# Kernel optimization log

Hardware: AMD Instinct MI355X
Metric: run time of the kernel (lower is better)

The kernel has to match this reference:

```python
import jax, jax.numpy as jnp
import numpy as np

EPS = 1e-7  # Keras K.epsilon()


def setup_inputs() -> dict:
    key = jax.random.key(0)
    k_x, k_w, k_b, k_u = jax.random.split(key, 4)
    B, T, D, A = 256, 512, 256, 50
    x = jax.random.normal(k_x, (B, T, D), dtype=jnp.float32)
    # Keras initializers.get('normal') -> stddev 0.05 RandomNormal
    W = jax.random.normal(k_w, (D, A), dtype=jnp.float32) * 0.05
    b = jax.random.normal(k_b, (A,), dtype=jnp.float32) * 0.05
    u = jax.random.normal(k_u, (A, 1), dtype=jnp.float32) * 0.05
    return {"x": x, "W": W, "b": b, "u": u}


def reference(x, W, b, u):
    # uit: [B, T, A]
    uit = jnp.tanh(jnp.einsum('btd,da->bta', x, W) + b)
    # ait: [B, T] raw scores -> exp-normalize (as in original, no max-subtract)
    ait = jnp.einsum('bta,a->bt', uit, u[:, 0])
    ait = jnp.exp(ait)
    ait = ait / (jnp.sum(ait, axis=1, keepdims=True) + EPS)
    # weighted pool over time: [B, D]
    return jnp.einsum('btd,bt->bd', x, ait)
```

## Files before the change

### kernel.cpp

```cpp
#include <hip/hip_runtime.h>
#include <hip/hip_bf16.h>
#include <math.h>

#define B_  256
#define T_  512
#define D_  256
#define A_  50
#define EPS 1e-7f
#define NW  16

typedef short  short8  __attribute__((ext_vector_type(8)));
typedef float  floatx4 __attribute__((ext_vector_type(4)));

__device__ inline unsigned short f2bf(float f) {
    unsigned int u = __float_as_uint(f);
    u = (u + 0x7fffu + ((u >> 16) & 1u)) >> 16;
    return (unsigned short)u;
}

__global__ void prep_kernel(const float* __restrict__ W,
                            const float* __restrict__ bias,
                            const float* __restrict__ u,
                            unsigned short* __restrict__ Wf,
                            float* __restrict__ bu64)
{
    int idx = blockIdx.x * 256 + threadIdx.x;
    int j  = idx & 7;
    int l  = (idx >> 3) & 63;
    int ks = (idx >> 9) & 7;
    int nt = idx >> 12;
    int n  = nt * 16 + (l & 15);
    int k  = ks * 32 + (l >> 4) * 8 + j;
    float val = (n < A_) ? W[k * A_ + n] : 0.0f;
    Wf[idx] = f2bf(val);
    if (idx < 64) {
        bu64[idx]      = (idx < A_) ? bias[idx] : 0.0f;
        bu64[64 + idx] = (idx < A_) ? u[idx]    : 0.0f;
    }
}

__device__ inline void pack_bf4(short8& av, int base, float fx, float fy,
                                float fz, float fw)
{
    union { __hip_bfloat162 h2; int i; } c0, c1;
    c0.h2 = __float22bfloat162_rn(make_float2(fx, fy));
    c1.h2 = __float22bfloat162_rn(make_float2(fz, fw));
    av[base + 0] = (short)(c0.i & 0xffff);
    av[base + 1] = (short)((unsigned)c0.i >> 16);
    av[base + 2] = (short)(c1.i & 0xffff);
    av[base + 3] = (short)((unsigned)c1.i >> 16);
}

__device__ inline float4 shflxor4(float4 v, int m) {
    return make_float4(__shfl_xor(v.x, m), __shfl_xor(v.y, m),
                       __shfl_xor(v.z, m), __shfl_xor(v.w, m));
}
__device__ inline float4 add4(float4 a, float4 b) {
    return make_float4(a.x + b.x, a.y + b.y, a.z + b.z, a.w + b.w);
}
__device__ inline float4 sel4(bool p, float4 a, float4 b) {
    return make_float4(p ? a.x : b.x, p ? a.y : b.y,
                       p ? a.z : b.z, p ? a.w : b.w);
}
__device__ inline float4 mul4s(float4 a, float s) {
    return make_float4(a.x * s, a.y * s, a.z * s, a.w * s);
}

__global__ __launch_bounds__(1024)
void fused_kernel(const float* __restrict__ x,
                  const unsigned short* __restrict__ Wf,
                  const float* __restrict__ bu64,
                  float* __restrict__ out)
{
    __shared__ int4  Wl[2048];
    __shared__ float s_lds[T_];
    __shared__ float part[NW * 256];
    __shared__ float s_inv;

    const int tid  = threadIdx.x;
    const int w    = tid >> 6;
    const int l    = tid & 63;
    const int c    = l & 15;
    const int quad = l >> 4;
    const int bb   = blockIdx.x;

    {
        const int4* __restrict__ wsrc = (const int4*)Wf;
        Wl[tid]        = wsrc[tid];
        Wl[tid + 1024] = wsrc[tid + 1024];
    }

    const float*  __restrict__ xb  = x + (size_t)bb * T_ * D_;
    const short8* __restrict__ wl8 = (const short8*)Wl;

    float bnc[4], unc[4];
    #pragma unroll
    for (int nt = 0; nt < 4; nt++) {
        bnc[nt] = bu64[nt * 16 + c];
        unc[nt] = bu64[64 + nt * 16 + c];
    }
    __syncthreads();

    float4 accp = make_float4(0.f, 0.f, 0.f, 0.f);

    #pragma unroll
    for (int t = 0; t < 2; t++) {
        const int rowbase = w * 32 + t * 16;
        const float4* __restrict__ xr =
            (const float4*)(xb + (size_t)(rowbase + c) * D_);

        floatx4 acc[4];
        #pragma unroll
        for (int nt = 0; nt < 4; nt++) acc[nt] = (floatx4){0.f, 0.f, 0.f, 0.f};

        #pragma unroll
        for (int ks = 0; ks < 8; ks++) {
            const float4 a0 = xr[8 * ks + 2 * quad];
            const float4 a1 = xr[8 * ks + 2 * quad + 1];
            short8 av;
            pack_bf4(av, 0, a0.x, a0.y, a0.z, a0.w);
            pack_bf4(av, 4, a1.x, a1.y, a1.z, a1.w);
            #pragma unroll
            for (int nt = 0; nt < 4; nt++) {
                const short8 bv = wl8[(nt * 8 + ks) * 64 + l];
                acc[nt] = __builtin_amdgcn_mfma_f32_16x16x32_bf16(av, bv, acc[nt], 0, 0, 0);
            }
        }

        #pragma unroll
        for (int r = 0; r < 4; r++) {
            float v = 0.0f;
            #pragma unroll
            for (int nt = 0; nt < 4; nt++)
                v += tanhf(acc[nt][r] + bnc[nt]) * unc[nt];
            #pragma unroll
            for (int off = 1; off < 16; off <<= 1)
                v += __shfl_xor(v, off, 16);
            if (c == 0)
                s_lds[rowbase + quad * 4 + r] = expf(v);
        }

        const float ec = s_lds[rowbase + c];

        float4 h8[8];
        #pragma unroll
        for (int j = 0; j < 8; j++) {
            const int o = (j >> 1) * 8 + quad * 2 + (j & 1);
            const float4 a = mul4s(xr[o],      ec);
            const float4 b = mul4s(xr[o + 32], ec);
            h8[j] = add4(sel4((c & 8) != 0, b, a),
                         shflxor4(sel4((c & 8) != 0, a, b), 8));
        }
        float4 h4[4];
        #pragma unroll
        for (int j = 0; j < 4; j++) {
            const float4 a = h4[0], bqq = h4[0];
            (void)a; (void)bqq;
            const float4 aa = h8[j], bb = h8[j + 4];
            h4[j] = add4(sel4((c & 4) != 0, bb, aa),
                         shflxor4(sel4((c & 4) != 0, aa, bb), 4));
        }
        float4 h2[2];
        #pragma unroll
        for (int j = 0; j < 2; j++) {
            const float4 aa = h4[j], bb = h4[j + 2];
            h2[j] = add4(sel4((c & 2) != 0, bb, aa),
                         shflxor4(sel4((c & 2) != 0, aa, bb), 2));
        }
        {
            const float4 aa = h2[0], bb = h2[1];
            const float4 h1 = add4(sel4((c & 1) != 0, bb, aa),
                                   shflxor4(sel4((c & 1) != 0, aa, bb), 1));
            accp = add4(accp, h1);
        }
    }

    const int g = (c >> 1) * 8 + quad * 2 + (c & 1);
    *(float4*)&part[w * 256 + g * 4] = accp;
    __syncthreads();

    if (tid < 64) {
        float s = 0.0f;
        #pragma unroll
        for (int k = 0; k < 8; k++) s += s_lds[tid + k * 64];
        #pragma unroll
        for (int off = 1; off < 64; off <<= 1) s += __shfl_xor(s, off);
        if (tid == 0) s_inv = 1.0f / (s + EPS);
    }
    __syncthreads();

    if (tid < 256) {
        float o = 0.0f;
        #pragma unroll
        for (int wv = 0; wv < NW; wv++) o += part[wv * 256 + tid];
        out[(size_t)bb * 256 + tid] = o * s_inv;
    }
}

extern "C" void kernel_launch(void* const* d_in, const int* in_sizes, int n_in,
                              void* d_out, int out_size, void* d_ws, size_t ws_size,
                              hipStream_t stream)
{
    const float* x = (const float*)d_in[0];
    const float* W = (const float*)d_in[1];
    const float* b = (const float*)d_in[2];
    const float* u = (const float*)d_in[3];

    unsigned short* Wf  = (unsigned short*)d_ws;
    float*         bu64 = (float*)(Wf + 16384);
    float*         out  = (float*)d_out;

    prep_kernel  <<<64,  256,  0, stream>>>(W, b, u, Wf, bu64);
    fused_kernel <<<B_,  1024, 0, stream>>>(x, Wf, bu64, out);
}
```

Baseline: 206.7 us.

## Split each batch row across two blocks with a combine kernel

The fused kernel now launches 512 blocks, each handling half of the time axis (256 rows) of one batch element. It writes the partial pooled vector and partial exp-sum to workspace. A new combine kernel adds the two halves and normalises. This is meant to raise occupancy and parallelism across the GPU's compute units (256 blocks left many idle), at the cost of an extra launch and a workspace round trip.

```diff
diff --git a/kernel.cpp b/kernel.cpp
--- a/kernel.cpp
+++ b/kernel.cpp
@@ -70,12 +70,12 @@
 void fused_kernel(const float* __restrict__ x,
                   const unsigned short* __restrict__ Wf,
                   const float* __restrict__ bu64,
-                  float* __restrict__ out)
+                  float* __restrict__ pp,
+                  float* __restrict__ ps)
 {
     __shared__ int4  Wl[2048];
-    __shared__ float s_lds[T_];
+    __shared__ float s_lds[256];
     __shared__ float part[NW * 256];
-    __shared__ float s_inv;
 
     const int tid  = threadIdx.x;
     const int w    = tid >> 6;
@@ -83,6 +83,8 @@
     const int c    = l & 15;
     const int quad = l >> 4;
     const int bb   = blockIdx.x;
+    const int bat  = bb >> 1;
+    const int half = bb & 1;
 
     {
         const int4* __restrict__ wsrc = (const int4*)Wf;
@@ -90,7 +92,7 @@
         Wl[tid + 1024] = wsrc[tid + 1024];
     }
 
-    const float*  __restrict__ xb  = x + (size_t)bb * T_ * D_;
+    const float*  __restrict__ xb  = x + (size_t)bat * T_ * D_;
     const short8* __restrict__ wl8 = (const short8*)Wl;
 
     float bnc[4], unc[4];
@@ -101,78 +103,71 @@
     }
     __syncthreads();
 
-    float4 accp = make_float4(0.f, 0.f, 0.f, 0.f);
-
-    #pragma unroll
-    for (int t = 0; t < 2; t++) {
-        const int rowbase = w * 32 + t * 16;
-        const float4* __restrict__ xr =
-            (const float4*)(xb + (size_t)(rowbase + c) * D_);
-
-        floatx4 acc[4];
-        #pragma unroll
-        for (int nt = 0; nt < 4; nt++) acc[nt] = (floatx4){0.f, 0.f, 0.f, 0.f};
-
-        #pragma unroll
-        for (int ks = 0; ks < 8; ks++) {
-            const float4 a0 = xr[8 * ks + 2 * quad];
-            const float4 a1 = xr[8 * ks + 2 * quad + 1];
-            short8 av;
-            pack_bf4(av, 0, a0.x, a0.y, a0.z, a0.w);
-            pack_bf4(av, 4, a1.x, a1.y, a1.z, a1.w);
-            #pragma unroll
-            for (int nt = 0; nt < 4; nt++) {
-                const short8 bv = wl8[(nt * 8 + ks) * 64 + l];
-                acc[nt] = __builtin_amdgcn_mfma_f32_16x16x32_bf16(av, bv, acc[nt], 0, 0, 0);
-            }
+    const int rowbase = w * 16;
+    const float4* __restrict__ xr =
+        (const float4*)(xb + (size_t)(half * 256 + rowbase + c) * D_);
+
+    floatx4 acc[4];
+    #pragma unroll
+    for (int nt = 0; nt < 4; nt++) acc[nt] = (floatx4){0.f, 0.f, 0.f, 0.f};
+
+    #pragma unroll
+    for (int ks = 0; ks < 8; ks++) {
+        const float4 a0 = xr[8 * ks + 2 * quad];
+        const float4 a1 = xr[8 * ks + 2 * quad + 1];
+        short8 av;
+        pack_bf4(av, 0, a0.x, a0.y, a0.z, a0.w);
+        pack_bf4(av, 4, a1.x, a1.y, a1.z, a1.w);
+        #pragma unroll
+        for (int nt = 0; nt < 4; nt++) {
+            const short8 bv = wl8[(nt * 8 + ks) * 64 + l];
+            acc[nt] = __builtin_amdgcn_mfma_f32_16x16x32_bf16(av, bv, acc[nt], 0, 0, 0);
         }
-
-        #pragma unroll
-        for (int r = 0; r < 4; r++) {
-            float v = 0.0f;
-            #pragma unroll
-            for (int nt = 0; nt < 4; nt++)
-                v += tanhf(acc[nt][r] + bnc[nt]) * unc[nt];
-            #pragma unroll
-            for (int off = 1; off < 16; off <<= 1)
-                v += __shfl_xor(v, off, 16);
-            if (c == 0)
-                s_lds[rowbase + quad * 4 + r] = expf(v);
-        }
-
-        const float ec = s_lds[rowbase + c];
-
-        float4 h8[8];
-        #pragma unroll
-        for (int j = 0; j < 8; j++) {
-            const int o = (j >> 1) * 8 + quad * 2 + (j & 1);
-            const float4 a = mul4s(xr[o],      ec);
-            const float4 b = mul4s(xr[o + 32], ec);
-            h8[j] = add4(sel4((c & 8) != 0, b, a),
-                         shflxor4(sel4((c & 8) != 0, a, b), 8));
-        }
-        float4 h4[4];
-        #pragma unroll
-        for (int j = 0; j < 4; j++) {
-            const float4 a = h4[0], bqq = h4[0];
-            (void)a; (void)bqq;
-            const float4 aa = h8[j], bb = h8[j + 4];
-            h4[j] = add4(sel4((c & 4) != 0, bb, aa),
-                         shflxor4(sel4((c & 4) != 0, aa, bb), 4));
-        }
-        float4 h2[2];
-        #pragma unroll
-        for (int j = 0; j < 2; j++) {
-            const float4 aa = h4[j], bb = h4[j + 2];
-            h2[j] = add4(sel4((c & 2) != 0, bb, aa),
-                         shflxor4(sel4((c & 2) != 0, aa, bb), 2));
-        }
-        {
-            const float4 aa = h2[0], bb = h2[1];
-            const float4 h1 = add4(sel4((c & 1) != 0, bb, aa),
-                                   shflxor4(sel4((c & 1) != 0, aa, bb), 1));
-            accp = add4(accp, h1);
-        }
+    }
+
+    #pragma unroll
+    for (int r = 0; r < 4; r++) {
+        float v = 0.0f;
+        #pragma unroll
+        for (int nt = 0; nt < 4; nt++)
+            v += tanhf(acc[nt][r] + bnc[nt]) * unc[nt];
+        #pragma unroll
+        for (int off = 1; off < 16; off <<= 1)
+            v += __shfl_xor(v, off, 16);
+        if (c == 0)
+            s_lds[rowbase + quad * 4 + r] = expf(v);
+    }
+
+    const float ec = s_lds[rowbase + c];
+
+    float4 h8[8];
+    #pragma unroll
+    for (int j = 0; j < 8; j++) {
+        const int o = (j >> 1) * 8 + quad * 2 + (j & 1);
+        const float4 a = mul4s(xr[o],      ec);
+        const float4 b = mul4s(xr[o + 32], ec);
+        h8[j] = add4(sel4((c & 8) != 0, b, a),
+                     shflxor4(sel4((c & 8) != 0, a, b), 8));
+    }
+    float4 h4[4];
+    #pragma unroll
+    for (int j = 0; j < 4; j++) {
+        const float4 aa = h8[j], bb = h8[j + 4];
+        h4[j] = add4(sel4((c & 4) != 0, bb, aa),
+                     shflxor4(sel4((c & 4) != 0, aa, bb), 4));
+    }
+    float4 h2[2];
+    #pragma unroll
+    for (int j = 0; j < 2; j++) {
+        const float4 aa = h4[j], bb = h4[j + 2];
+        h2[j] = add4(sel4((c & 2) != 0, bb, aa),
+                     shflxor4(sel4((c & 2) != 0, aa, bb), 2));
+    }
+    float4 accp;
+    {
+        const float4 aa = h2[0], bb = h2[1];
+        accp = add4(sel4((c & 1) != 0, bb, aa),
+                    shflxor4(sel4((c & 1) != 0, aa, bb), 1));
     }
 
     const int g = (c >> 1) * 8 + quad * 2 + (c & 1);
@@ -182,19 +177,31 @@
     if (tid < 64) {
         float s = 0.0f;
         #pragma unroll
-        for (int k = 0; k < 8; k++) s += s_lds[tid + k * 64];
+        for (int k = 0; k < 4; k++) s += s_lds[tid + k * 64];
         #pragma unroll
         for (int off = 1; off < 64; off <<= 1) s += __shfl_xor(s, off);
-        if (tid == 0) s_inv = 1.0f / (s + EPS);
-    }
-    __syncthreads();
+        if (tid == 0) ps[bb] = s;
+    }
 
     if (tid < 256) {
         float o = 0.0f;
         #pragma unroll
         for (int wv = 0; wv < NW; wv++) o += part[wv * 256 + tid];
-        out[(size_t)bb * 256 + tid] = o * s_inv;
-    }
+        pp[(size_t)bb * 256 + tid] = o;
+    }
+}
+
+__global__ __launch_bounds__(256)
+void combine_kernel(const float* __restrict__ pp,
+                    const float* __restrict__ ps,
+                    float* __restrict__ out)
+{
+    const int b = blockIdx.x;
+    const int d = threadIdx.x;
+    const float inv = 1.0f / (ps[2 * b] + ps[2 * b + 1] + EPS);
+    const float v = pp[(size_t)(2 * b) * 256 + d] +
+                    pp[(size_t)(2 * b + 1) * 256 + d];
+    out[(size_t)b * 256 + d] = v * inv;
 }
 
 extern "C" void kernel_launch(void* const* d_in, const int* in_sizes, int n_in,
@@ -206,10 +213,13 @@
     const float* b = (const float*)d_in[2];
     const float* u = (const float*)d_in[3];
 
-    unsigned short* Wf  = (unsigned short*)d_ws;
-    float*         bu64 = (float*)(Wf + 16384);
-    float*         out  = (float*)d_out;
-
-    prep_kernel  <<<64,  256,  0, stream>>>(W, b, u, Wf, bu64);
-    fused_kernel <<<B_,  1024, 0, stream>>>(x, Wf, bu64, out);
-}
+    unsigned short* Wf   = (unsigned short*)d_ws;
+    float*          bu64 = (float*)(Wf + 16384);
+    float*          pp   = bu64 + 128;
+    float*          ps   = pp + 512 * 256;
+    float*          out  = (float*)d_out;
+
+    prep_kernel    <<<64,  256,  0, stream>>>(W, b, u, Wf, bu64);
+    fused_kernel   <<<512, 1024, 0, stream>>>(x, Wf, bu64, pp, ps);
+    combine_kernel <<<256, 256,  0, stream>>>(pp, ps, out);
+}
```

Result: slower. 217.0 us (+5.0%).
